# Performance work log

Measured on AMD Instinct MI355X. Metric: run time of the kernel, lower is better.

The kernel has to match this reference:

```python
import jax, jax.numpy as jnp
import numpy as np

BATCH = 8
TABLE_NUM = 16          # levels L
TABLE_DIM = 8192        # entries per table
RES_MIN, RES_MAX = 16, 256
SAMPLE_RES = 256
N = SAMPLE_RES * SAMPLE_RES
CH = TABLE_NUM * 2      # feature dim per level is 2
STYLE_DIM = 512
PRIME = np.uint32(2654435761)
LN_EPS = 1e-5
DEMOD_EPS = 1e-8

# geometric level resolutions (Instant-NGP style)
_b = np.exp((np.log(RES_MAX) - np.log(RES_MIN)) / (TABLE_NUM - 1))
RES_LIST = [int(np.floor(RES_MIN * (_b ** l))) for l in range(TABLE_NUM)]


def _corner_idx_weights(coords):
    """coords [N,2] in [0,1] -> (idx [L,N,4] int32 flat into L*T, w [L,N,4])."""
    idx_all, w_all = [], []
    for l, res in enumerate(RES_LIST):
        pos = coords * (res - 1)                     # [N,2]
        p0f = jnp.floor(pos)
        frac = pos - p0f                              # bilinear fractions
        p0 = jnp.clip(p0f.astype(jnp.int32), 0, res - 2)
        x0, y0 = p0[:, 0], p0[:, 1]
        x1, y1 = x0 + 1, y0 + 1
        fx, fy = frac[:, 0], frac[:, 1]
        cx = jnp.stack([x0, x1, x0, x1], -1)          # [N,4]
        cy = jnp.stack([y0, y0, y1, y1], -1)
        w = jnp.stack([(1 - fx) * (1 - fy), fx * (1 - fy),
                       (1 - fx) * fy, fx * fy], -1)   # [N,4]
        if res * res <= TABLE_DIM:                    # dense grid fits: direct index
            idx = cy * res + cx
        else:                                         # spatial hash
            h = cx.astype(jnp.uint32) ^ (cy.astype(jnp.uint32) * PRIME)
            idx = (h % jnp.uint32(TABLE_DIM)).astype(jnp.int32)
        idx_all.append(idx + l * TABLE_DIM)
        w_all.append(w)
    return jnp.stack(idx_all), jnp.stack(w_all)       # [L,N,4]


def _hash_retrieve(tables, idx, w):
    """tables [B,L,T,2] -> bilinear multi-res lookup [B,N,2L]."""
    B = tables.shape[0]
    tf = tables.reshape(B, TABLE_NUM * TABLE_DIM, 2)
    g = tf[:, idx.reshape(-1)]                        # [B, L*N*4, 2]
    g = g.reshape(B, TABLE_NUM, N, 4, 2)
    feats = jnp.einsum('blncf,lnc->blnf', g, w)       # [B,L,N,2]
    return feats.transpose(0, 2, 1, 3).reshape(B, N, CH)


def _hash_recon(tokens, idx, w):
    """tokens [B,N,2L] -> transpose scatter back into tables [B,L,T,2]."""
    B = tokens.shape[0]
    t = tokens.reshape(B, N, TABLE_NUM, 2).transpose(0, 2, 1, 3)   # [B,L,N,2]
    contrib = jnp.einsum('blnf,lnc->blncf', t, w)                   # [B,L,N,4,2]
    out = jnp.zeros((B, TABLE_NUM * TABLE_DIM, 2), tokens.dtype)
    out = out.at[:, idx.reshape(-1)].add(contrib.reshape(B, -1, 2))
    return out.reshape(B, TABLE_NUM, TABLE_DIM, 2)


def _synthesis_layer(x, s, affine_w, affine_b, conv_w, conv_b):
    """StyleGAN2 modulated 3x3 conv (demodulate, up=1) + bias + lrelu*sqrt(2)."""
    styles = s @ (affine_w.T / np.sqrt(STYLE_DIM)) + affine_b       # [B,ch]
    xm = x * styles[:, :, None, None]                               # modulate input
    y = jax.lax.conv_general_dilated(xm, conv_w, (1, 1), [(1, 1), (1, 1)],
                                     dimension_numbers=('NCHW', 'OIHW', 'NCHW'))
    # demod coef: rsqrt(sum_{i,k,l} (w_oikl * style_i)^2 + eps)
    dcoef = jax.lax.rsqrt(jnp.einsum('oikl,bi->bo', conv_w * conv_w,
                                     styles * styles) + DEMOD_EPS)
    y = y * dcoef[:, :, None, None] + conv_b[None, :, None, None]
    return jax.nn.leaky_relu(y, 0.2) * np.sqrt(2.0)


def setup_inputs() -> dict:
    key = jax.random.key(0)
    k1, k2, k3, k4 = jax.random.split(key, 4)
    inputs = jax.random.normal(k1, (BATCH, TABLE_NUM, 2 * TABLE_DIM), jnp.float32)
    s = jax.random.normal(k2, (BATCH, STYLE_DIM), jnp.float32)
    g = jnp.linspace(0.0, 1.0, SAMPLE_RES)
    yy, xx = jnp.meshgrid(g, g, indexing='ij')
    coords = jnp.stack([xx, yy], -1).reshape(N, 2).astype(jnp.float32)
    affine_w = jax.random.normal(k3, (CH, STYLE_DIM), jnp.float32)
    affine_b = jnp.ones((CH,), jnp.float32)          # bias_init=1
    conv_w = jax.random.normal(k4, (CH, CH, 3, 3), jnp.float32)
    conv_b = jnp.zeros((CH,), jnp.float32)
    return {"inputs": inputs, "s": s, "coords": coords,
            "affine_w": affine_w, "affine_b": affine_b,
            "conv_w": conv_w, "conv_b": conv_b}


def reference(inputs, s, coords, affine_w, affine_b, conv_w, conv_b):
    B = inputs.shape[0]
    tables = inputs.reshape(B, TABLE_NUM, TABLE_DIM, 2)
    idx, w = _corner_idx_weights(coords)
    feats = _hash_retrieve(tables, idx, w)                 # [B,N,ch]
    block = feats.reshape(B, SAMPLE_RES, SAMPLE_RES, CH).transpose(0, 3, 1, 2)
    block = _synthesis_layer(block, s, affine_w, affine_b, conv_w, conv_b)
    tokens = block.reshape(B, CH, N).transpose(0, 2, 1)    # [B,N,ch]
    recon = _hash_recon(tokens, idx, w)                    # [B,L,T,2]
    out = recon.reshape(B, TABLE_NUM, -1) + inputs         # residual
    mu = out.mean(-1, keepdims=True)
    var = ((out - mu) ** 2).mean(-1, keepdims=True)
    return (out - mu) * jax.lax.rsqrt(var + LN_EPS)        # layer_norm, no affine
```

## Files before the change

### kernel.cpp

```cpp
#include <hip/hip_runtime.h>
#include <hip/hip_fp16.h>
#include <cmath>
#include <cstdint>

#define NB 8
#define NL 16
#define TD 8192
#define NPIX 65536
#define CH 32
#define SD 512

static constexpr uint32_t PRIME = 2654435761u;

typedef __attribute__((ext_vector_type(8))) short bf16x8;
typedef __attribute__((ext_vector_type(4))) float f32x4;

static constexpr int cNCX[16] = {4,5,5,5,6,6,7,7,8,9,10,12,13,15,18,20};
static constexpr int CTOFF[17] = {0,16,41,66,91,127,163,212,261,325,406,506,650,819,1044,1368,1768};

struct LevelParams {
    int res[NL];
    int hashed[NL];
    int uoff[NL];
    int soff[NL];
    int cwoff[NL];
    int nck[NL];
    int sumr;
    int nwaves;
};

__device__ __forceinline__ unsigned short f2bf(float f) {
    uint32_t u = __float_as_uint(f);
    return (unsigned short)((u + 0x7fffu + ((u >> 16) & 1u)) >> 16);
}
__device__ __forceinline__ float bflo(uint32_t u) { return __uint_as_float(u << 16); }
__device__ __forceinline__ float bfhi(uint32_t u) { return __uint_as_float(u & 0xffff0000u); }
__device__ __forceinline__ uint32_t packbf(float a, float b) {
    return (uint32_t)f2bf(a) | ((uint32_t)f2bf(b) << 16);
}
__device__ __forceinline__ uint32_t packh2(float a, float b) {
    return (uint32_t)__half_as_ushort(__float2half_rn(a)) |
           ((uint32_t)__half_as_ushort(__float2half_rn(b)) << 16);
}
__device__ __forceinline__ float h2lo(uint32_t u) {
    return __half2float(__ushort_as_half((unsigned short)(u & 0xffffu)));
}
__device__ __forceinline__ float h2hi(uint32_t u) {
    return __half2float(__ushort_as_half((unsigned short)(u >> 16)));
}

__global__ __launch_bounds__(256) void k_prep(
    const float* __restrict__ s, const float* __restrict__ aw,
    const float* __restrict__ ab, const float* __restrict__ cw,
    const float* __restrict__ coords,
    float* __restrict__ styles, float* __restrict__ dcoef,
    int* __restrict__ ctab, float* __restrict__ ftab, int* __restrict__ stab,
    unsigned short* __restrict__ wpack, LevelParams p) {
    int bb = blockIdx.x;
    int t = threadIdx.x;
    if (bb < NB) {
        int b = bb;
        int c = t >> 3, part = t & 7;
        const float* sv = s + b * SD + part * 64;
        const float* wv = aw + c * SD + part * 64;
        float acc = 0.f;
        #pragma unroll 8
        for (int k = 0; k < 64; ++k) acc += sv[k] * wv[k];
        acc += __shfl_xor(acc, 1, 64);
        acc += __shfl_xor(acc, 2, 64);
        acc += __shfl_xor(acc, 4, 64);
        __shared__ float st_sh[CH];
        if (part == 0) {
            float st = acc * 0.04419417382415922f  + ab[c];
            styles[b * CH + c] = st;
            st_sh[c] = st;
        }
        __syncthreads();
        if (t < CH) {
            float d = 0.f;
            for (int i = 0; i < CH; ++i) {
                const float* w9 = cw + (t * CH + i) * 9;
                float ws = 0.f;
                #pragma unroll
                for (int k = 0; k < 9; ++k) ws += w9[k] * w9[k];
                float si = st_sh[i];
                d += ws * si * si;
            }
            dcoef[b * CH + t] = rsqrtf(d + 1e-8f);
        }
    } else if (bb < NB + NL) {
        int l = bb - NB;
        int j = t;
        int r = p.res[l];
        float g = coords[2 * j];
        float px = g * (float)(r - 1);
        float fl = floorf(px);
        float f = px - fl;
        int c = min((int)fl, r - 2);
        ctab[l * 256 + j] = c;
        ftab[l * 256 + j] = f;
        __shared__ int cs[256];
        cs[j] = c;
        __syncthreads();
        for (int cc = j; cc <= r; cc += 256) {
            int cnt = 0;
            for (int i = 0; i < 256; ++i) cnt += (cs[i] < cc) ? 1 : 0;
            stab[p.soff[l] + cc] = cnt;
        }
    } else {
        int idx = (bb - NB - NL) * 256 + t;
        if (idx < 9 * 4 * 32 * 8) {
            int j = idx & 7;
            int o = (idx >> 3) & 31;
            int kgi = (idx >> 8) & 3;
            int tap = idx >> 10;
            wpack[idx] = f2bf(cw[(o * 32 + kgi * 8 + j) * 9 + tap]);
        }
    }
}

template<int L>
__device__ __forceinline__ uint32_t feat1p(float2 cv, float2 rv, const uint32_t* ctile) {
    int a = CTOFF[L] + __float_as_int(rv.x) * cNCX[L] + __float_as_int(cv.x);
    float fx = cv.y, fy = rv.y;
    uint32_t c00 = ctile[a], c10 = ctile[a + 1];
    uint32_t c01 = ctile[a + cNCX[L]], c11 = ctile[a + cNCX[L] + 1];
    float w00 = (1.f - fx) * (1.f - fy), w10 = fx * (1.f - fy);
    float w01 = (1.f - fx) * fy,         w11 = fx * fy;
    float f0 = w00 * bflo(c00) + w10 * bflo(c10) + w01 * bflo(c01) + w11 * bflo(c11);
    float f1 = w00 * bfhi(c00) + w10 * bfhi(c10) + w01 * bfhi(c01) + w11 * bfhi(c11);
    return packbf(f0, f1);
}

template<int L0>
__device__ __forceinline__ void phase1(int lane, int tx0, int ty0,
                                       const float2* col2, const float2* row2,
                                       const uint32_t* ctile, uint32_t* xt) {
    constexpr int q = L0 / 4;
    #pragma unroll
    for (int it = 0; it < 6; ++it) {
        int pl = it * 64 + lane;
        int rr = pl / 18, cc = pl - rr * 18;
        int gy = ty0 + rr - 1, gx = tx0 + cc - 1;
        uint4 v = make_uint4(0u, 0u, 0u, 0u);
        if (pl < 324 && (unsigned)gy < 256u && (unsigned)gx < 256u) {
            float2 cv0 = col2[(L0 + 0) * 18 + cc], rv0 = row2[(L0 + 0) * 18 + rr];
            float2 cv1 = col2[(L0 + 1) * 18 + cc], rv1 = row2[(L0 + 1) * 18 + rr];
            float2 cv2 = col2[(L0 + 2) * 18 + cc], rv2 = row2[(L0 + 2) * 18 + rr];
            float2 cv3 = col2[(L0 + 3) * 18 + cc], rv3 = row2[(L0 + 3) * 18 + rr];
            v.x = feat1p<L0 + 0>(cv0, rv0, ctile);
            v.y = feat1p<L0 + 1>(cv1, rv1, ctile);
            v.z = feat1p<L0 + 2>(cv2, rv2, ctile);
            v.w = feat1p<L0 + 3>(cv3, rv3, ctile);
        }
        if (pl < 324)
            *(uint4*)(xt + (size_t)(pl * 4 + (q ^ (cc & 3))) * 4) = v;
    }
}

__global__ __launch_bounds__(256) void k_conv(
    const float* __restrict__ tables, const int* __restrict__ ctab,
    const float* __restrict__ ftab, const float* __restrict__ styles,
    const unsigned short* __restrict__ wpack, const float* __restrict__ cb,
    const float* __restrict__ dcoef, uint32_t* __restrict__ tokens,
    LevelParams p) {
    __shared__ uint32_t xt[18 * 18 * 16];
    __shared__ uint32_t ctile[1768];
    __shared__ float2 col2[NL * 18];
    __shared__ float2 row2[NL * 18];
    __shared__ int cxbase[NL], cybase[NL], ncxA[NL], ncyA[NL];

    int bid = blockIdx.x;
    int b = bid & 7;
    int t = bid >> 3;
    int tx0 = (t & 15) * 16, ty0 = (t >> 4) * 16;
    int tid = threadIdx.x;
    int lane = tid & 63, wv = tid >> 6;
    int npx = lane & 15, kg = lane >> 4;
    const float* tb = tables + (size_t)b * NL * TD * 2;

    if (tid < NL) {
        int l = tid;
        int cxb = ctab[l * 256 + max(tx0 - 1, 0)];
        int cyb = ctab[l * 256 + max(ty0 - 1, 0)];
        cxbase[l] = cxb;
        cybase[l] = cyb;
        ncxA[l] = ctab[l * 256 + min(tx0 + 16, 255)] - cxb + 2;
        ncyA[l] = ctab[l * 256 + min(ty0 + 16, 255)] - cyb + 2;
    }
    __syncthreads();

    for (int u0 = tid; u0 < NL * 36; u0 += 256) {
        int l = u0 / 36, pos = u0 - l * 36;
        if (pos < 18) {
            int gx = tx0 - 1 + pos;
            int gxc = min(max(gx, 0), 255);
            col2[l * 18 + pos] = make_float2(
                __int_as_float(ctab[l * 256 + gxc] - cxbase[l]), ftab[l * 256 + gxc]);
        } else {
            int pr = pos - 18;
            int gy = ty0 - 1 + pr;
            int gyc = min(max(gy, 0), 255);
            row2[l * 18 + pr] = make_float2(
                __int_as_float(ctab[l * 256 + gyc] - cybase[l]), ftab[l * 256 + gyc]);
        }
    }

    #pragma unroll
    for (int l = 0; l < NL; ++l) {
        const int NCXl = cNCX[l];
        const int CAP = (CTOFF[l + 1] - CTOFF[l]);
        float s0 = styles[b * CH + 2 * l], s1 = styles[b * CH + 2 * l + 1];
        for (int u2 = tid; u2 < CAP; u2 += 256) {
            int sy = u2 / NCXl;
            int sx = u2 - sy * NCXl;
            if (sx < ncxA[l] && sy < ncyA[l]) {
                int ax = cxbase[l] + sx, ay = cybase[l] + sy;
                int r = p.res[l];
                uint32_t idx = p.hashed[l]
                    ? (((uint32_t)ax ^ ((uint32_t)ay * PRIME)) & (TD - 1))
                    : (uint32_t)(ay * r + ax);
                float2 g = *(const float2*)(tb + (size_t)l * TD * 2 + 2 * idx);
                ctile[CTOFF[l] + sy * NCXl + sx] = packbf(g.x * s0, g.y * s1);
            }
        }
    }
    __syncthreads();

    switch (wv) {
        case 0: phase1<0>(lane, tx0, ty0, col2, row2, ctile, xt); break;
        case 1: phase1<4>(lane, tx0, ty0, col2, row2, ctile, xt); break;
        case 2: phase1<8>(lane, tx0, ty0, col2, row2, ctile, xt); break;
        default: phase1<12>(lane, tx0, ty0, col2, row2, ctile, xt); break;
    }
    __builtin_amdgcn_sched_barrier(0);

    bf16x8 wf[9][2];
    #pragma unroll
    for (int tp = 0; tp < 9; ++tp) {
        wf[tp][0] = *(const bf16x8*)(wpack + (size_t)((tp * 4 + kg) * 32 + npx) * 8);
        wf[tp][1] = *(const bf16x8*)(wpack + (size_t)((tp * 4 + kg) * 32 + 16 + npx) * 8);
    }
    float dc[2][4], bs[2][4];
    #pragma unroll
    for (int ob = 0; ob < 2; ++ob)
        #pragma unroll
        for (int rg = 0; rg < 4; ++rg) {
            int oc = ob * 16 + kg * 4 + rg;
            dc[ob][rg] = dcoef[b * CH + oc];
            bs[ob][rg] = cb[oc];
        }
    __syncthreads();

    #pragma unroll 1
    for (int it = 0; it < 4; ++it) {
        int py_l = it * 4 + wv;
        int px_l = npx;
        f32x4 a0 = {0.f, 0.f, 0.f, 0.f};
        f32x4 a1 = {0.f, 0.f, 0.f, 0.f};
        #pragma unroll
        for (int ky = 0; ky < 3; ++ky) {
            int rowb = (py_l + ky) * 18;
            #pragma unroll
            for (int kx = 0; kx < 3; ++kx) {
                int cc = px_l + kx;
                bf16x8 bf = *(const bf16x8*)(xt + (((rowb + cc) << 2) + (kg ^ (cc & 3))) * 4);
                a0 = __builtin_amdgcn_mfma_f32_16x16x32_bf16(wf[ky * 3 + kx][0], bf, a0, 0, 0, 0);
                a1 = __builtin_amdgcn_mfma_f32_16x16x32_bf16(wf[ky * 3 + kx][1], bf, a1, 0, 0, 0);
            }
        }
        int py = ty0 + py_l, px = tx0 + px_l;
        size_t pbase = (size_t)py * 256 + px;
        {
            float y0 = a0[0] * dc[0][0] + bs[0][0];
            float y1 = a0[1] * dc[0][1] + bs[0][1];
            float y2 = a0[2] * dc[0][2] + bs[0][2];
            float y3 = a0[3] * dc[0][3] + bs[0][3];
            y0 = (y0 > 0.f ? y0 : 0.2f * y0) * 1.4142135623730951f;
            y1 = (y1 > 0.f ? y1 : 0.2f * y1) * 1.4142135623730951f;
            y2 = (y2 > 0.f ? y2 : 0.2f * y2) * 1.4142135623730951f;
            y3 = (y3 > 0.f ? y3 : 0.2f * y3) * 1.4142135623730951f;
            int lp0 = kg * 2;
            tokens[((size_t)(b * NL + lp0)) * NPIX + pbase] = packbf(y0, y1);
            tokens[((size_t)(b * NL + lp0 + 1)) * NPIX + pbase] = packbf(y2, y3);
        }
        {
            float y0 = a1[0] * dc[1][0] + bs[1][0];
            float y1 = a1[1] * dc[1][1] + bs[1][1];
            float y2 = a1[2] * dc[1][2] + bs[1][2];
            float y3 = a1[3] * dc[1][3] + bs[1][3];
            y0 = (y0 > 0.f ? y0 : 0.2f * y0) * 1.4142135623730951f;
            y1 = (y1 > 0.f ? y1 : 0.2f * y1) * 1.4142135623730951f;
            y2 = (y2 > 0.f ? y2 : 0.2f * y2) * 1.4142135623730951f;
            y3 = (y3 > 0.f ? y3 : 0.2f * y3) * 1.4142135623730951f;
            int lp0 = 8 + kg * 2;
            tokens[((size_t)(b * NL + lp0)) * NPIX + pbase] = packbf(y0, y1);
            tokens[((size_t)(b * NL + lp0 + 1)) * NPIX + pbase] = packbf(y2, y3);
        }
    }
}

__global__ __launch_bounds__(256) void k_recon1(const uint32_t* __restrict__ tokens,
                                                const int* __restrict__ ctab,
                                                const float* __restrict__ ftab,
                                                const int* __restrict__ stab,
                                                uint32_t* __restrict__ U, LevelParams p) {
    __shared__ float2 cf[256];
    __shared__ int sl[260];
    __shared__ uint32_t tok[4][256];
    int l = blockIdx.x >> 6;
    int grp = blockIdx.x & 63;
    int b = blockIdx.y;
    int tid = threadIdx.x;
    int lane = tid & 63, wv = tid >> 6;
    int r = p.res[l];

    cf[tid] = make_float2(__int_as_float(ctab[l * 256 + tid]), ftab[l * 256 + tid]);
    for (int q = tid; q <= r; q += 256) sl[q] = stab[p.soff[l] + q];
    int i = grp * 4 + wv;
    const uint32_t* trow = tokens + (size_t)(b * NL + l) * NPIX + i * 256;
    *(uint4*)&tok[wv][lane * 4] = *(const uint4*)(trow + lane * 4);
    __syncthreads();

    uint32_t* Ul = U + (size_t)b * (p.sumr * 256) + p.uoff[l] + (size_t)i * r;
    int nck = p.nck[l];
    #pragma unroll 1
    for (int ck = 0; ck < nck; ++ck) {
        int cx = ck * 64 + lane;
        bool valid = cx < r;
        int jlo = 0, jhi = -1;
        if (valid) {
            jlo = (cx > 0) ? sl[cx - 1] : 0;
            jhi = sl[min(cx + 1, r)] - 1;
        }
        float a0 = 0.f, a1 = 0.f;
        for (int j = jlo; j <= jhi; ++j) {
            float2 cfv = cf[j];
            int c = __float_as_int(cfv.x);
            float f = cfv.y;
            float w = (c == cx) ? (1.f - f) : f;
            uint32_t tv = tok[wv][j];
            a0 += w * bflo(tv);
            a1 += w * bfhi(tv);
        }
        if (valid)
            Ul[cx] = packh2(a0, a1);
    }
}

__global__ __launch_bounds__(256) void k_recon2(const uint32_t* __restrict__ U,
                                                const int* __restrict__ ctab,
                                                const float* __restrict__ ftab,
                                                const int* __restrict__ stab,
                                                float* __restrict__ R, LevelParams p) {
    int wid = blockIdx.x * 4 + (threadIdx.x >> 6);
    int lane = threadIdx.x & 63;
    int b = blockIdx.y;
    if (wid >= p.nwaves) return;
    int l = 0;
    #pragma unroll
    for (int q = 1; q < NL; ++q) if (wid >= p.cwoff[q]) l = q;
    int u = wid - p.cwoff[l];
    int r = p.res[l];
    int nck = p.nck[l];
    int cy = u / nck;
    int ck = u - cy * nck;
    int cx = ck * 64 + lane;
    bool valid = cx < r;
    const int* Sl = stab + p.soff[l];
    int ilo = (cy > 0) ? Sl[cy - 1] : 0;
    int ihi = Sl[min(cy + 1, r)] - 1;
    const uint32_t* Ub = U + (size_t)b * (p.sumr * 256) + p.uoff[l];
    const int* crow = ctab + l * 256;
    const float* frow = ftab + l * 256;
    float a0 = 0.f, a1 = 0.f;
    for (int i = ilo; i <= ihi; ++i) {
        int c = crow[i];
        float f = frow[i];
        float w = (c == cy) ? (1.f - f) : f;
        if (valid) {
            uint32_t uu = Ub[(size_t)i * r + cx];
            a0 += w * h2lo(uu);
            a1 += w * h2hi(uu);
        }
    }
    if (!valid) return;
    float* Rbl = R + (size_t)(b * NL + l) * TD * 2;
    if (p.hashed[l]) {
        uint32_t h = ((uint32_t)cx ^ ((uint32_t)cy * PRIME)) & (TD - 1);
        atomicAdd(&Rbl[2 * h], a0);
        atomicAdd(&Rbl[2 * h + 1], a1);
    } else {
        *(float2*)(Rbl + 2 * (cy * r + cx)) = make_float2(a0, a1);
    }
}

__global__ __launch_bounds__(512) void k_ln(const float* __restrict__ R,
                                            const float* __restrict__ inp,
                                            float* __restrict__ out) {
    int row = blockIdx.x;
    const float4* rv = (const float4*)(R + (size_t)row * 16384);
    const float4* iv = (const float4*)(inp + (size_t)row * 16384);
    int tid = threadIdx.x;
    float sum = 0.f, ssq = 0.f;
    for (int k = tid; k < 4096; k += 512) {
        float4 a = rv[k], c = iv[k];
        float x0 = a.x + c.x, x1 = a.y + c.y, x2 = a.z + c.z, x3 = a.w + c.w;
        sum += x0 + x1 + x2 + x3;
        ssq += x0 * x0 + x1 * x1 + x2 * x2 + x3 * x3;
    }
    #pragma unroll
    for (int off = 32; off > 0; off >>= 1) {
        sum += __shfl_xor(sum, off, 64);
        ssq += __shfl_xor(ssq, off, 64);
    }
    __shared__ float red[16];
    int w = tid >> 6;
    if ((tid & 63) == 0) { red[w * 2] = sum; red[w * 2 + 1] = ssq; }
    __syncthreads();
    sum = 0.f; ssq = 0.f;
    #pragma unroll
    for (int q = 0; q < 8; ++q) { sum += red[q * 2]; ssq += red[q * 2 + 1]; }
    float mu = sum * (1.f / 16384.f);
    float var = ssq * (1.f / 16384.f) - mu * mu;
    float inv = rsqrtf(var + 1e-5f);
    float4* ob = (float4*)(out + (size_t)row * 16384);
    for (int k = tid; k < 4096; k += 512) {
        float4 a = rv[k], c = iv[k];
        float4 o4;
        o4.x = (a.x + c.x - mu) * inv;
        o4.y = (a.y + c.y - mu) * inv;
        o4.z = (a.z + c.z - mu) * inv;
        o4.w = (a.w + c.w - mu) * inv;
        ob[k] = o4;
    }
}

extern "C" void kernel_launch(void* const* d_in, const int* in_sizes, int n_in,
                              void* d_out, int out_size, void* d_ws, size_t ws_size,
                              hipStream_t stream) {
    const float* inputs = (const float*)d_in[0];
    const float* s      = (const float*)d_in[1];
    const float* coords = (const float*)d_in[2];
    const float* aw     = (const float*)d_in[3];
    const float* ab     = (const float*)d_in[4];
    const float* cw     = (const float*)d_in[5];
    const float* cb     = (const float*)d_in[6];

    char* ws = (char*)d_ws;
    uint32_t* U      = (uint32_t*)(ws);
    uint32_t* tokens = (uint32_t*)(ws + 33554432);
    float*    R      = (float*)(ws + 67108864);
    float*    styles = (float*)(ws + 75497472);
    float*    dcoef  = (float*)(ws + 75498496);
    int*      ctab   = (int*)(ws + 75499520);
    float*    ftab   = (float*)(ws + 75515904);
    int*      stab   = (int*)(ws + 75532288);
    unsigned short* wpack = (unsigned short*)(ws + 75540480);

    LevelParams p;
    double bb = exp((log(256.0) - log(16.0)) / 15.0);
    int uoff = 0, soff = 0, cwoff = 0, sumr = 0;
    for (int l = 0; l < NL; ++l) {
        int r = (int)floor(16.0 * pow(bb, (double)l));
        p.res[l] = r;
        p.hashed[l] = (r * r > TD) ? 1 : 0;
        p.uoff[l] = uoff;
        p.soff[l] = soff;
        p.cwoff[l] = cwoff;
        int nck = (r + 63) >> 6;
        p.nck[l] = nck;
        uoff += r * 256;
        soff += r + 2;
        cwoff += r * nck;
        sumr += r;
    }
    p.sumr = sumr;
    p.nwaves = cwoff;

    hipMemsetAsync(R, 0, (size_t)NB * NL * TD * 2 * sizeof(float), stream);
    hipLaunchKernelGGL(k_prep, dim3(NB + NL + 36), dim3(256), 0, stream,
                       s, aw, ab, cw, coords, styles, dcoef, ctab, ftab, stab, wpack, p);
    hipLaunchKernelGGL(k_conv, dim3(2048), dim3(256), 0, stream,
                       inputs, ctab, ftab, styles, wpack, cb, dcoef, tokens, p);
    hipLaunchKernelGGL(k_recon1, dim3(NL * 64, NB), dim3(256), 0, stream,
                       tokens, ctab, ftab, stab, U, p);
    hipLaunchKernelGGL(k_recon2, dim3((p.nwaves + 3) / 4, NB), dim3(256), 0, stream,
                       U, ctab, ftab, stab, R, p);
    hipLaunchKernelGGL(k_ln, dim3(NB * NL), dim3(512), 0, stream,
                       R, inputs, (float*)d_out);
}
```

Before: 111.0 us.

## Process two batch items per conv block to amortize setup and weight loads

Each k_conv block now handles one spatial tile for two batch items instead of one, and the grid is halved. The per-tile index setup (cxbase/col2/row2), conv weight fragments and bias loads are shared across both batches, and both batches' table gathers are issued together. In exchange, shared memory for the corner tile doubles, the block count drops to 1024, and phase1 plus the MFMA loop run serially twice with extra barriers.

```diff
diff --git a/kernel.cpp b/kernel.cpp
--- a/kernel.cpp
+++ b/kernel.cpp
@@ -165,19 +165,21 @@
     const float* __restrict__ dcoef, uint32_t* __restrict__ tokens,
     LevelParams p) {
     __shared__ uint32_t xt[18 * 18 * 16];
-    __shared__ uint32_t ctile[1768];
+    __shared__ uint32_t ctile2[2][1768];
     __shared__ float2 col2[NL * 18];
     __shared__ float2 row2[NL * 18];
     __shared__ int cxbase[NL], cybase[NL], ncxA[NL], ncyA[NL];
 
     int bid = blockIdx.x;
-    int b = bid & 7;
-    int t = bid >> 3;
+    int pb = bid & 3;
+    int t = bid >> 2;
+    int b0 = pb * 2;
     int tx0 = (t & 15) * 16, ty0 = (t >> 4) * 16;
     int tid = threadIdx.x;
     int lane = tid & 63, wv = tid >> 6;
     int npx = lane & 15, kg = lane >> 4;
-    const float* tb = tables + (size_t)b * NL * TD * 2;
+    const float* tbA = tables + (size_t)b0 * NL * TD * 2;
+    const float* tbB = tbA + (size_t)NL * TD * 2;
 
     if (tid < NL) {
         int l = tid;
@@ -210,7 +212,8 @@
     for (int l = 0; l < NL; ++l) {
         const int NCXl = cNCX[l];
         const int CAP = (CTOFF[l + 1] - CTOFF[l]);
-        float s0 = styles[b * CH + 2 * l], s1 = styles[b * CH + 2 * l + 1];
+        float sA0 = styles[b0 * CH + 2 * l],       sA1 = styles[b0 * CH + 2 * l + 1];
+        float sB0 = styles[(b0 + 1) * CH + 2 * l], sB1 = styles[(b0 + 1) * CH + 2 * l + 1];
         for (int u2 = tid; u2 < CAP; u2 += 256) {
             int sy = u2 / NCXl;
             int sx = u2 - sy * NCXl;
@@ -220,20 +223,13 @@
                 uint32_t idx = p.hashed[l]
                     ? (((uint32_t)ax ^ ((uint32_t)ay * PRIME)) & (TD - 1))
                     : (uint32_t)(ay * r + ax);
-                float2 g = *(const float2*)(tb + (size_t)l * TD * 2 + 2 * idx);
-                ctile[CTOFF[l] + sy * NCXl + sx] = packbf(g.x * s0, g.y * s1);
+                float2 gA = *(const float2*)(tbA + (size_t)l * TD * 2 + 2 * idx);
+                float2 gB = *(const float2*)(tbB + (size_t)l * TD * 2 + 2 * idx);
+                ctile2[0][CTOFF[l] + sy * NCXl + sx] = packbf(gA.x * sA0, gA.y * sA1);
+                ctile2[1][CTOFF[l] + sy * NCXl + sx] = packbf(gB.x * sB0, gB.y * sB1);
             }
         }
     }
-    __syncthreads();
-
-    switch (wv) {
-        case 0: phase1<0>(lane, tx0, ty0, col2, row2, ctile, xt); break;
-        case 1: phase1<4>(lane, tx0, ty0, col2, row2, ctile, xt); break;
-        case 2: phase1<8>(lane, tx0, ty0, col2, row2, ctile, xt); break;
-        default: phase1<12>(lane, tx0, ty0, col2, row2, ctile, xt); break;
-    }
-    __builtin_amdgcn_sched_barrier(0);
 
     bf16x8 wf[9][2];
     #pragma unroll
@@ -241,62 +237,83 @@
         wf[tp][0] = *(const bf16x8*)(wpack + (size_t)((tp * 4 + kg) * 32 + npx) * 8);
         wf[tp][1] = *(const bf16x8*)(wpack + (size_t)((tp * 4 + kg) * 32 + 16 + npx) * 8);
     }
-    float dc[2][4], bs[2][4];
+    float bs[2][4];
+    #pragma unroll
+    for (int ob = 0; ob < 2; ++ob)
+        #pragma unroll
+        for (int rg = 0; rg < 4; ++rg)
+            bs[ob][rg] = cb[ob * 16 + kg * 4 + rg];
+    float dcA[2][4], dcB[2][4];
     #pragma unroll
     for (int ob = 0; ob < 2; ++ob)
         #pragma unroll
         for (int rg = 0; rg < 4; ++rg) {
             int oc = ob * 16 + kg * 4 + rg;
-            dc[ob][rg] = dcoef[b * CH + oc];
-            bs[ob][rg] = cb[oc];
+            dcA[ob][rg] = dcoef[b0 * CH + oc];
+            dcB[ob][rg] = dcoef[(b0 + 1) * CH + oc];
         }
     __syncthreads();
 
-    #pragma unroll 1
-    for (int it = 0; it < 4; ++it) {
-        int py_l = it * 4 + wv;
-        int px_l = npx;
-        f32x4 a0 = {0.f, 0.f, 0.f, 0.f};
-        f32x4 a1 = {0.f, 0.f, 0.f, 0.f};
-        #pragma unroll
-        for (int ky = 0; ky < 3; ++ky) {
-            int rowb = (py_l + ky) * 18;
+    #pragma unroll
+    for (int bb = 0; bb < 2; ++bb) {
+        int b = b0 + bb;
+        const uint32_t* ct = ctile2[bb];
+        switch (wv) {
+            case 0: phase1<0>(lane, tx0, ty0, col2, row2, ct, xt); break;
+            case 1: phase1<4>(lane, tx0, ty0, col2, row2, ct, xt); break;
+            case 2: phase1<8>(lane, tx0, ty0, col2, row2, ct, xt); break;
+            default: phase1<12>(lane, tx0, ty0, col2, row2, ct, xt); break;
+        }
+        __syncthreads();
+
+        #pragma unroll 1
+        for (int it = 0; it < 4; ++it) {
+            int py_l = it * 4 + wv;
+            int px_l = npx;
+            f32x4 a0 = {0.f, 0.f, 0.f, 0.f};
+            f32x4 a1 = {0.f, 0.f, 0.f, 0.f};
             #pragma unroll
-            for (int kx = 0; kx < 3; ++kx) {
-                int cc = px_l + kx;
-                bf16x8 bf = *(const bf16x8*)(xt + (((rowb + cc) << 2) + (kg ^ (cc & 3))) * 4);
-                a0 = __builtin_amdgcn_mfma_f32_16x16x32_bf16(wf[ky * 3 + kx][0], bf, a0, 0, 0, 0);
-                a1 = __builtin_amdgcn_mfma_f32_16x16x32_bf16(wf[ky * 3 + kx][1], bf, a1, 0, 0, 0);
+            for (int ky = 0; ky < 3; ++ky) {
+                int rowb = (py_l + ky) * 18;
+                #pragma unroll
+                for (int kx = 0; kx < 3; ++kx) {
+                    int cc = px_l + kx;
+                    bf16x8 bf = *(const bf16x8*)(xt + (((rowb + cc) << 2) + (kg ^ (cc & 3))) * 4);
+                    a0 = __builtin_amdgcn_mfma_f32_16x16x32_bf16(wf[ky * 3 + kx][0], bf, a0, 0, 0, 0);
+                    a1 = __builtin_amdgcn_mfma_f32_16x16x32_bf16(wf[ky * 3 + kx][1], bf, a1, 0, 0, 0);
+                }
             }
-        }
-        int py = ty0 + py_l, px = tx0 + px_l;
-        size_t pbase = (size_t)py * 256 + px;
-        {
-            float y0 = a0[0] * dc[0][0] + bs[0][0];
-            float y1 = a0[1] * dc[0][1] + bs[0][1];
-            float y2 = a0[2] * dc[0][2] + bs[0][2];
-            float y3 = a0[3] * dc[0][3] + bs[0][3];
-            y0 = (y0 > 0.f ? y0 : 0.2f * y0) * 1.4142135623730951f;
-            y1 = (y1 > 0.f ? y1 : 0.2f * y1) * 1.4142135623730951f;
-            y2 = (y2 > 0.f ? y2 : 0.2f * y2) * 1.4142135623730951f;
-            y3 = (y3 > 0.f ? y3 : 0.2f * y3) * 1.4142135623730951f;
-            int lp0 = kg * 2;
-            tokens[((size_t)(b * NL + lp0)) * NPIX + pbase] = packbf(y0, y1);
-            tokens[((size_t)(b * NL + lp0 + 1)) * NPIX + pbase] = packbf(y2, y3);
-        }
-        {
-            float y0 = a1[0] * dc[1][0] + bs[1][0];
-            float y1 = a1[1] * dc[1][1] + bs[1][1];
-            float y2 = a1[2] * dc[1][2] + bs[1][2];
-            float y3 = a1[3] * dc[1][3] + bs[1][3];
-            y0 = (y0 > 0.f ? y0 : 0.2f * y0) * 1.4142135623730951f;
-            y1 = (y1 > 0.f ? y1 : 0.2f * y1) * 1.4142135623730951f;
-            y2 = (y2 > 0.f ? y2 : 0.2f * y2) * 1.4142135623730951f;
-            y3 = (y3 > 0.f ? y3 : 0.2f * y3) * 1.4142135623730951f;
-            int lp0 = 8 + kg * 2;
-            tokens[((size_t)(b * NL + lp0)) * NPIX + pbase] = packbf(y0, y1);
-            tokens[((size_t)(b * NL + lp0 + 1)) * NPIX + pbase] = packbf(y2, y3);
-        }
+            int py = ty0 + py_l, px = tx0 + px_l;
+            size_t pbase = (size_t)py * 256 + px;
+            const float (*dc)[4] = bb ? dcB : dcA;
+            {
+                float y0 = a0[0] * dc[0][0] + bs[0][0];
+                float y1 = a0[1] * dc[0][1] + bs[0][1];
+                float y2 = a0[2] * dc[0][2] + bs[0][2];
+                float y3 = a0[3] * dc[0][3] + bs[0][3];
+                y0 = (y0 > 0.f ? y0 : 0.2f * y0) * 1.4142135623730951f;
+                y1 = (y1 > 0.f ? y1 : 0.2f * y1) * 1.4142135623730951f;
+                y2 = (y2 > 0.f ? y2 : 0.2f * y2) * 1.4142135623730951f;
+                y3 = (y3 > 0.f ? y3 : 0.2f * y3) * 1.4142135623730951f;
+                int lp0 = kg * 2;
+                tokens[((size_t)(b * NL + lp0)) * NPIX + pbase] = packbf(y0, y1);
+                tokens[((size_t)(b * NL + lp0 + 1)) * NPIX + pbase] = packbf(y2, y3);
+            }
+            {
+                float y0 = a1[0] * dc[1][0] + bs[1][0];
+                float y1 = a1[1] * dc[1][1] + bs[1][1];
+                float y2 = a1[2] * dc[1][2] + bs[1][2];
+                float y3 = a1[3] * dc[1][3] + bs[1][3];
+                y0 = (y0 > 0.f ? y0 : 0.2f * y0) * 1.4142135623730951f;
+                y1 = (y1 > 0.f ? y1 : 0.2f * y1) * 1.4142135623730951f;
+                y2 = (y2 > 0.f ? y2 : 0.2f * y2) * 1.4142135623730951f;
+                y3 = (y3 > 0.f ? y3 : 0.2f * y3) * 1.4142135623730951f;
+                int lp0 = 8 + kg * 2;
+                tokens[((size_t)(b * NL + lp0)) * NPIX + pbase] = packbf(y0, y1);
+                tokens[((size_t)(b * NL + lp0 + 1)) * NPIX + pbase] = packbf(y2, y3);
+            }
+        }
+        __syncthreads();
     }
 }
 
@@ -481,7 +498,7 @@
     hipMemsetAsync(R, 0, (size_t)NB * NL * TD * 2 * sizeof(float), stream);
     hipLaunchKernelGGL(k_prep, dim3(NB + NL + 36), dim3(256), 0, stream,
                        s, aw, ab, cw, coords, styles, dcoef, ctab, ftab, stab, wpack, p);
-    hipLaunchKernelGGL(k_conv, dim3(2048), dim3(256), 0, stream,
+    hipLaunchKernelGGL(k_conv, dim3(1024), dim3(256), 0, stream,
                        inputs, ctab, ftab, styles, wpack, cb, dcoef, tokens, p);
     hipLaunchKernelGGL(k_recon1, dim3(NL * 64, NB), dim3(256), 0, stream,
                        tokens, ctab, ftab, stab, U, p);
```

Measured after the change: 121.4 us. +9.4%, slower.

## Split hash-table corner gather into a separate kernel staging tiles in global memory

Applied to the files above, without the earlier changes.

Moves the per-tile random gather of hashed table corners (with style scaling and bf16 packing) out of the conv kernel into a new k_gather kernel that writes packed, padded tiles to workspace. The conv kernel then loads each tile with coalesced 16-byte copies instead of doing scattered latency-bound loads before its compute phase. This adds an extra kernel launch and a global write plus read of roughly 14 MB, in exchange for a leaner conv prologue.

```diff
diff --git a/kernel.cpp b/kernel.cpp
--- a/kernel.cpp
+++ b/kernel.cpp
@@ -119,6 +119,51 @@
     }
 }
 
+__global__ __launch_bounds__(256) void k_gather(
+    const float* __restrict__ tables, const int* __restrict__ ctab,
+    const float* __restrict__ styles, uint32_t* __restrict__ ctileG,
+    LevelParams p) {
+    __shared__ int cxbase[NL], cybase[NL], ncxA[NL], ncyA[NL];
+    int bid = blockIdx.x;
+    int b = bid & 7;
+    int t = bid >> 3;
+    int tx0 = (t & 15) * 16, ty0 = (t >> 4) * 16;
+    int tid = threadIdx.x;
+    const float* tb = tables + (size_t)b * NL * TD * 2;
+    if (tid < NL) {
+        int l = tid;
+        int cxb = ctab[l * 256 + max(tx0 - 1, 0)];
+        int cyb = ctab[l * 256 + max(ty0 - 1, 0)];
+        cxbase[l] = cxb;
+        cybase[l] = cyb;
+        ncxA[l] = ctab[l * 256 + min(tx0 + 16, 255)] - cxb + 2;
+        ncyA[l] = ctab[l * 256 + min(ty0 + 16, 255)] - cyb + 2;
+    }
+    __syncthreads();
+    uint32_t* out = ctileG + (size_t)bid * 1768;
+    #pragma unroll
+    for (int l = 0; l < NL; ++l) {
+        const int NCXl = cNCX[l];
+        const int CAP = (CTOFF[l + 1] - CTOFF[l]);
+        float s0 = styles[b * CH + 2 * l], s1 = styles[b * CH + 2 * l + 1];
+        for (int u2 = tid; u2 < CAP; u2 += 256) {
+            int sy = u2 / NCXl;
+            int sx = u2 - sy * NCXl;
+            uint32_t val = 0u;
+            if (sx < ncxA[l] && sy < ncyA[l]) {
+                int ax = cxbase[l] + sx, ay = cybase[l] + sy;
+                int r = p.res[l];
+                uint32_t idx = p.hashed[l]
+                    ? (((uint32_t)ax ^ ((uint32_t)ay * PRIME)) & (TD - 1))
+                    : (uint32_t)(ay * r + ax);
+                float2 g = *(const float2*)(tb + (size_t)l * TD * 2 + 2 * idx);
+                val = packbf(g.x * s0, g.y * s1);
+            }
+            out[CTOFF[l] + u2] = val;
+        }
+    }
+}
+
 template<int L>
 __device__ __forceinline__ uint32_t feat1p(float2 cv, float2 rv, const uint32_t* ctile) {
     int a = CTOFF[L] + __float_as_int(rv.x) * cNCX[L] + __float_as_int(cv.x);
@@ -159,8 +204,8 @@
 }
 
 __global__ __launch_bounds__(256) void k_conv(
-    const float* __restrict__ tables, const int* __restrict__ ctab,
-    const float* __restrict__ ftab, const float* __restrict__ styles,
+    const uint32_t* __restrict__ ctileG, const int* __restrict__ ctab,
+    const float* __restrict__ ftab,
     const unsigned short* __restrict__ wpack, const float* __restrict__ cb,
     const float* __restrict__ dcoef, uint32_t* __restrict__ tokens,
     LevelParams p) {
@@ -168,7 +213,7 @@
     __shared__ uint32_t ctile[1768];
     __shared__ float2 col2[NL * 18];
     __shared__ float2 row2[NL * 18];
-    __shared__ int cxbase[NL], cybase[NL], ncxA[NL], ncyA[NL];
+    __shared__ int cxbase[NL], cybase[NL];
 
     int bid = blockIdx.x;
     int b = bid & 7;
@@ -177,19 +222,18 @@
     int tid = threadIdx.x;
     int lane = tid & 63, wv = tid >> 6;
     int npx = lane & 15, kg = lane >> 4;
-    const float* tb = tables + (size_t)b * NL * TD * 2;
 
     if (tid < NL) {
         int l = tid;
-        int cxb = ctab[l * 256 + max(tx0 - 1, 0)];
-        int cyb = ctab[l * 256 + max(ty0 - 1, 0)];
-        cxbase[l] = cxb;
-        cybase[l] = cyb;
-        ncxA[l] = ctab[l * 256 + min(tx0 + 16, 255)] - cxb + 2;
-        ncyA[l] = ctab[l * 256 + min(ty0 + 16, 255)] - cyb + 2;
+        cxbase[l] = ctab[l * 256 + max(tx0 - 1, 0)];
+        cybase[l] = ctab[l * 256 + max(ty0 - 1, 0)];
+    }
+    {
+        const uint4* src = (const uint4*)(ctileG + (size_t)bid * 1768);
+        for (int i = tid; i < 442; i += 256)
+            *(uint4*)(ctile + i * 4) = src[i];
     }
     __syncthreads();
-
     for (int u0 = tid; u0 < NL * 36; u0 += 256) {
         int l = u0 / 36, pos = u0 - l * 36;
         if (pos < 18) {
@@ -203,26 +247,6 @@
             int gyc = min(max(gy, 0), 255);
             row2[l * 18 + pr] = make_float2(
                 __int_as_float(ctab[l * 256 + gyc] - cybase[l]), ftab[l * 256 + gyc]);
-        }
-    }
-
-    #pragma unroll
-    for (int l = 0; l < NL; ++l) {
-        const int NCXl = cNCX[l];
-        const int CAP = (CTOFF[l + 1] - CTOFF[l]);
-        float s0 = styles[b * CH + 2 * l], s1 = styles[b * CH + 2 * l + 1];
-        for (int u2 = tid; u2 < CAP; u2 += 256) {
-            int sy = u2 / NCXl;
-            int sx = u2 - sy * NCXl;
-            if (sx < ncxA[l] && sy < ncyA[l]) {
-                int ax = cxbase[l] + sx, ay = cybase[l] + sy;
-                int r = p.res[l];
-                uint32_t idx = p.hashed[l]
-                    ? (((uint32_t)ax ^ ((uint32_t)ay * PRIME)) & (TD - 1))
-                    : (uint32_t)(ay * r + ax);
-                float2 g = *(const float2*)(tb + (size_t)l * TD * 2 + 2 * idx);
-                ctile[CTOFF[l] + sy * NCXl + sx] = packbf(g.x * s0, g.y * s1);
-            }
         }
     }
     __syncthreads();
@@ -449,6 +473,7 @@
 
     char* ws = (char*)d_ws;
     uint32_t* U      = (uint32_t*)(ws);
+    uint32_t* ctileG = (uint32_t*)(ws + 16777216);
     uint32_t* tokens = (uint32_t*)(ws + 33554432);
     float*    R      = (float*)(ws + 67108864);
     float*    styles = (float*)(ws + 75497472);
@@ -481,8 +506,10 @@
     hipMemsetAsync(R, 0, (size_t)NB * NL * TD * 2 * sizeof(float), stream);
     hipLaunchKernelGGL(k_prep, dim3(NB + NL + 36), dim3(256), 0, stream,
                        s, aw, ab, cw, coords, styles, dcoef, ctab, ftab, stab, wpack, p);
+    hipLaunchKernelGGL(k_gather, dim3(2048), dim3(256), 0, stream,
+                       inputs, ctab, styles, ctileG, p);
     hipLaunchKernelGGL(k_conv, dim3(2048), dim3(256), 0, stream,
-                       inputs, ctab, ftab, styles, wpack, cb, dcoef, tokens, p);
+                       ctileG, ctab, ftab, wpack, cb, dcoef, tokens, p);
     hipLaunchKernelGGL(k_recon1, dim3(NL * 64, NB), dim3(256), 0, stream,
                        tokens, ctab, ftab, stab, U, p);
     hipLaunchKernelGGL(k_recon2, dim3((p.nwaves + 3) / 4, NB), dim3(256), 0, stream,
```

New measurement: 110.1 us. About the same (-0.8%).
